# Kernel tuning notes

Hardware: AMD Instinct MI355X
Metric: run time of the kernel (lower is better)

## Reference

```python
import jax, jax.numpy as jnp
import numpy as np

B = 65536      # batch
FDIM = 256     # features_dim (flatten extractor => obs dim)
ADIM = 8       # action dim
T = 3          # n_tasks
H = 256        # net_arch width
IN = FDIM + ADIM

_PARAM_SHAPES = [("W1", (T, IN, H)), ("b1", (T, H)), ("W2", (T, H, H)), ("b2", (T, H)),
                 ("W3", (T, H, H)), ("b3", (T, H)), ("W4", (T, H, 1)), ("b4", (T, 1))]

def setup_inputs() -> dict:
    key = jax.random.key(0)
    ks = jax.random.split(key, 2 + 2 * len(_PARAM_SHAPES))
    d = {"obs": jax.random.normal(ks[0], (B, FDIM), dtype=jnp.float32),
         "actions": jax.random.normal(ks[1], (B, ADIM), dtype=jnp.float32)}
    i = 2
    for q in ("q1", "q2"):
        for name, sh in _PARAM_SHAPES:
            d[f"{q}_{name}"] = jax.random.normal(ks[i], sh, dtype=jnp.float32) * 0.05
            i += 1
    return d

def _heads(x, W1, b1, W2, b2, W3, b3, W4, b4):
    # x: [B, IN]; per-task stacked MLP -> [T, B]
    h = jax.nn.relu(jnp.einsum('bi,tih->tbh', x, W1) + b1[:, None, :])
    h = jax.nn.relu(jnp.einsum('tbh,thk->tbk', h, W2) + b2[:, None, :])
    h = jax.nn.relu(jnp.einsum('tbh,thk->tbk', h, W3) + b3[:, None, :])
    return (jnp.einsum('tbh,tho->tbo', h, W4) + b4[:, None, :])[..., 0]

def reference(obs, actions,
              q1_W1, q1_b1, q1_W2, q1_b2, q1_W3, q1_b3, q1_W4, q1_b4,
              q2_W1, q2_b1, q2_W2, q2_b2, q2_W3, q2_b3, q2_W4, q2_b4):
    x = jnp.concatenate([obs, actions], axis=1)           # [B, IN]
    task = jnp.argmax(obs[:, -T:], axis=-1)               # [B] hard top-1 routing
    mask = jax.nn.one_hot(task, T, dtype=x.dtype).T       # [T, B]
    y1 = _heads(x, q1_W1, q1_b1, q1_W2, q1_b2, q1_W3, q1_b3, q1_W4, q1_b4)  # [T, B]
    y2 = _heads(x, q2_W1, q2_b1, q2_W2, q2_b2, q2_W3, q2_b3, q2_W4, q2_b4)
    q1 = jnp.sum(y1 * mask, axis=0)[:, None]              # [B, 1]
    q2 = jnp.sum(y2 * mask, axis=0)[:, None]
    return (q1, q2)
```

## Files before the change

### kernel.cpp

```cpp
#include <hip/hip_runtime.h>
#include <hip/hip_bf16.h>


#define NB 65536
#define MROWS 48
#define XSTR 296
#define HSTR 264

typedef __attribute__((ext_vector_type(8))) short short8;
typedef __attribute__((ext_vector_type(4))) short short4v;
typedef __attribute__((ext_vector_type(4))) float f32x4;

__device__ __forceinline__ float bf2f(unsigned short u){
  union { unsigned int i; float f; } x; x.i = ((unsigned int)u) << 16; return x.f;
}
__device__ __forceinline__ unsigned short f2bf(float f){
  unsigned int x = __float_as_uint(f);
  x += 0x7fffu + ((x >> 16) & 1u);
  return (unsigned short)(x >> 16);
}
__device__ __forceinline__ float ldval(const void* p, int idx, int isbf16){
  return isbf16 ? bf2f(((const unsigned short*)p)[idx]) : ((const float*)p)[idx];
}

__device__ __forceinline__ int block_sniff(const void* obs, int tid, int* sflag){
  if (tid < 64) {
    unsigned short u = ((const unsigned short*)obs)[tid * 2];
    int e = (u >> 7) & 0xFF;
    unsigned long long m = __ballot(e >= 110 && e <= 132);
    if (tid == 0) *sflag = (__popcll(m) >= 32) ? 1 : 0;
  }
  __syncthreads();
  return *sflag;
}

struct KParams {
  const void* obs;
  const void* act;
  const unsigned short* w1t[2];
  const unsigned short* w2t[2];
  const unsigned short* w3t[2];
  const void* b1[2];
  const void* b2[2];
  const void* b3[2];
  const void* w4[2];
  const void* b4[2];
  const int* counts;
  const int* perm;
  void* out;
};

__device__ __forceinline__ int task_of(const void* obs, int b, int isbf16){
  float v0, v1, v2;
  if (isbf16) {
    short4v u = *(const short4v*)((const unsigned short*)obs + b * 256 + 252);
    v0 = bf2f((unsigned short)u[1]); v1 = bf2f((unsigned short)u[2]); v2 = bf2f((unsigned short)u[3]);
  } else {
    f32x4 u = *(const f32x4*)((const float*)obs + b * 256 + 252);
    v0 = u[1]; v1 = u[2]; v2 = u[3];
  }
  int t = 0; float m = v0;
  if (v1 > m) { m = v1; t = 1; }
  if (v2 > m) { t = 2; }
  return t;
}

__global__ void prep_count(const void* q1W1, const void* q1W2, const void* q1W3,
                           const void* q2W1, const void* q2W2, const void* q2W3,
                           const void* obs, unsigned short* out,
                           int* hist, unsigned char* tasks){
  __shared__ int sflag;
  int tid = threadIdx.x;
  int isbf16 = block_sniff(obs, tid, &sflag);
  if (blockIdx.x >= 600) {
    __shared__ int h[3];
    if (tid < 3) h[tid] = 0;
    __syncthreads();
    int blk = blockIdx.x - 600;
    int b = blk * 256 + tid;
    int t = task_of(obs, b, isbf16);
    tasks[b] = (unsigned char)t;
    atomicAdd(&h[t], 1);
    __syncthreads();
    if (tid < 3) hist[blk * 3 + tid] = h[tid];
    return;
  }
  int gid8 = (blockIdx.x * 256 + tid) * 8;
  int net = gid8 / 614400;
  int idx = gid8 - net * 614400;
  const void* W1 = net ? q2W1 : q1W1;
  const void* W2 = net ? q2W2 : q1W2;
  const void* W3 = net ? q2W3 : q1W3;
  short8 sv;
  if (idx < 221184) {
    int t = idx / 73728; int i = idx - t * 73728;
    int g = i / 4608;  int r = i - g * 4608;
    int kb = r >> 9;   int q2 = r & 511;
    int l16 = q2 >> 5; int rem = q2 & 31;
    int n = g * 16 + l16;
    int k = kb * 32 + (rem & ~7);
    #pragma unroll
    for (int j = 0; j < 8; j++) {
      int kk = k + j;
      sv[j] = (kk < 264) ? (short)f2bf(ldval(W1, (t * 264 + kk) * 256 + n, isbf16)) : (short)0;
    }
  } else if (idx < 417792) {
    int j0 = idx - 221184;
    int t = j0 >> 16; int i = j0 & 65535;
    int g = i >> 12;  int r = i & 4095;
    int kb = r >> 9;  int q2 = r & 511;
    int l16 = q2 >> 5; int rem = q2 & 31;
    int n = g * 16 + l16;
    int k = kb * 32 + (rem & ~7);
    #pragma unroll
    for (int j = 0; j < 8; j++)
      sv[j] = (short)f2bf(ldval(W2, t * 65536 + (k + j) * 256 + n, isbf16));
  } else {
    int j0 = idx - 417792;
    int t = j0 >> 16; int i = j0 & 65535;
    int g = i >> 12;  int r = i & 4095;
    int kb = r >> 9;  int q2 = r & 511;
    int l16 = q2 >> 5; int rem = q2 & 31;
    int n = g * 16 + l16;
    int k = kb * 32 + (rem & ~7);
    #pragma unroll
    for (int j = 0; j < 8; j++)
      sv[j] = (short)f2bf(ldval(W3, t * 65536 + (k + j) * 256 + n, isbf16));
  }
  *(short8*)(out + net * 614400 + idx) = sv;
}

__global__ void route_scatter(const unsigned char* __restrict__ tasks,
                              const int* __restrict__ hist,
                              int* counts, int* perm){
  __shared__ int sh[3][256];
  __shared__ int totals[3], pres[3], base[3], zz[3];
  int tid = threadIdx.x;
  int blk = blockIdx.x;
  sh[0][tid] = hist[tid * 3 + 0];
  sh[1][tid] = hist[tid * 3 + 1];
  sh[2][tid] = hist[tid * 3 + 2];
  if (tid < 3) zz[tid] = 0;
  __syncthreads();
  if (tid < 3) {
    int tot = 0, pre = 0;
    for (int b = 0; b < 256; b++) {
      int v = sh[tid][b];
      if (b < blk) pre += v;
      tot += v;
    }
    totals[tid] = tot; pres[tid] = pre;
  }
  __syncthreads();
  if (tid < 3) {
    int a0 = ((totals[0] + MROWS - 1) / MROWS) * MROWS;
    int a1 = ((totals[1] + MROWS - 1) / MROWS) * MROWS;
    int off = (tid == 0) ? 0 : (tid == 1) ? a0 : a0 + a1;
    base[tid] = off + pres[tid];
    if (blk == 0) counts[tid] = totals[tid];
  }
  __syncthreads();
  int b = blk * 256 + tid;
  int t = tasks[b];
  int r = atomicAdd(&zz[t], 1);
  perm[base[t] + r] = b;
}

template<int KC>
__device__ __forceinline__ void run_layer(const unsigned short* __restrict__ lin, int lstride,
                                          const unsigned short* __restrict__ wt,
                                          const void* bias, unsigned short* lout,
                                          int isbf16, int wave, int quad, int l16, int nbase){
  const unsigned short* wg = wt + (wave * 2) * (KC * 512) + l16 * 32 + quad * 8;
  short8 bfr[KC][2];
  #pragma unroll
  for (int kb = 0; kb < KC; ++kb) {
    bfr[kb][0] = *(const short8*)(wg + kb * 512);
    bfr[kb][1] = *(const short8*)(wg + KC * 512 + kb * 512);
  }
  f32x4 acc[3][2] = {};
  #pragma unroll
  for (int kb = 0; kb < KC; ++kb) {
    short8 afr[3];
    int ko = kb * 32 + quad * 8;
    #pragma unroll
    for (int mt = 0; mt < 3; mt++)
      afr[mt] = *(const short8*)(lin + (mt * 16 + l16) * lstride + ko);
    #pragma unroll
    for (int mt = 0; mt < 3; mt++)
      #pragma unroll
      for (int nt = 0; nt < 2; nt++)
        acc[mt][nt] = __builtin_amdgcn_mfma_f32_16x16x32_bf16(afr[mt], bfr[kb][nt], acc[mt][nt], 0, 0, 0);
  }
  float bv[2];
  #pragma unroll
  for (int nt = 0; nt < 2; nt++) bv[nt] = ldval(bias, nbase + nt * 16 + l16, isbf16);
  #pragma unroll
  for (int mt = 0; mt < 3; mt++)
    #pragma unroll
    for (int nt = 0; nt < 2; nt++) {
      f32x4 a = acc[mt][nt];
      #pragma unroll
      for (int r = 0; r < 4; r++) {
        float v = fmaxf(a[r] + bv[nt], 0.f);
        lout[(mt * 16 + quad * 4 + r) * HSTR + nbase + nt * 16 + l16] = f2bf(v);
      }
    }
  __syncthreads();
}

__global__ __launch_bounds__(512, 6) void fused_kernel(KParams p){
  __shared__ unsigned short X[MROWS * XSTR];
  __shared__ unsigned short HA[MROWS * HSTR];
  unsigned short* HB = X;
  int* sflag = (int*)HA;

  int tid = threadIdx.x;
  int net = blockIdx.y;
  int p0  = blockIdx.x * MROWS;
  int isbf16 = block_sniff(p.obs, tid, sflag);
  int c0 = p.counts[0], c1 = p.counts[1], c2 = p.counts[2];
  int off1 = ((c0 + MROWS - 1) / MROWS) * MROWS;
  int off2 = off1 + ((c1 + MROWS - 1) / MROWS) * MROWS;
  int task  = (p0 >= off2) ? 2 : ((p0 >= off1) ? 1 : 0);
  int segend = (task == 0) ? c0 : (task == 1) ? off1 + c1 : off2 + c2;

  if (tid < MROWS * 8) {
    int srow = tid >> 3, seg = tid & 7;
    int pos = p0 + srow;
    int r = (pos < segend) ? p.perm[pos] : -1;
    #pragma unroll
    for (int j = 0; j < 5; ++j) {
      int c = seg + 8 * j;
      if (c <= 35) {
        short8 sv = {0,0,0,0,0,0,0,0};
        if (r >= 0 && c < 33) {
          if (isbf16) {
            const unsigned short* src = (c < 32) ? ((const unsigned short*)p.obs + r * 256 + c * 8)
                                                 : ((const unsigned short*)p.act + r * 8);
            sv = *(const short8*)src;
          } else {
            const float* src = (c < 32) ? ((const float*)p.obs + r * 256 + c * 8)
                                        : ((const float*)p.act + r * 8);
            f32x4 a = *(const f32x4*)src;
            f32x4 b = *(const f32x4*)(src + 4);
            #pragma unroll
            for (int q = 0; q < 4; q++) { sv[q] = (short)f2bf(a[q]); sv[4 + q] = (short)f2bf(b[q]); }
          }
        }
        *(short8*)(X + srow * XSTR + c * 8) = sv;
      }
    }
  }
  __syncthreads();

  int wave = tid >> 6, lane = tid & 63, quad = lane >> 4, l16 = lane & 15;
  int nbase = wave * 32;

  int bsz = isbf16 ? 2 : 4;
  run_layer<9>(X,  XSTR, p.w1t[net] + task * 73728, (const char*)p.b1[net] + task * 256 * bsz, HA, isbf16, wave, quad, l16, nbase);
  run_layer<8>(HA, HSTR, p.w2t[net] + task * 65536, (const char*)p.b2[net] + task * 256 * bsz, HB, isbf16, wave, quad, l16, nbase);
  run_layer<8>(HB, HSTR, p.w3t[net] + task * 65536, (const char*)p.b3[net] + task * 256 * bsz, HA, isbf16, wave, quad, l16, nbase);

  if (tid < MROWS * 8) {
    int row = tid >> 3, seg = tid & 7;
    float s = 0.f;
    #pragma unroll
    for (int kk = 0; kk < 32; kk += 8) {
      short8 hv = *(const short8*)(HA + row * HSTR + seg * 32 + kk);
      float wv[8];
      if (isbf16) {
        const unsigned short* w4p = (const unsigned short*)p.w4[net] + task * 256 + seg * 32 + kk;
        short8 t = *(const short8*)w4p;
        #pragma unroll
        for (int j = 0; j < 8; j++) wv[j] = bf2f((unsigned short)t[j]);
      } else {
        const float* w4p = (const float*)p.w4[net] + task * 256 + seg * 32 + kk;
        f32x4 a = *(const f32x4*)w4p;
        f32x4 b = *(const f32x4*)(w4p + 4);
        #pragma unroll
        for (int j = 0; j < 4; j++) { wv[j] = a[j]; wv[4 + j] = b[j]; }
      }
      #pragma unroll
      for (int j = 0; j < 8; j++)
        s += bf2f((unsigned short)hv[j]) * wv[j];
    }
    s += __shfl_xor(s, 1);
    s += __shfl_xor(s, 2);
    s += __shfl_xor(s, 4);
    if (seg == 0) {
      int pos = p0 + row;
      if (pos < segend) {
        int r = p.perm[pos];
        float y = s + ldval(p.b4[net], task, isbf16);
        if (isbf16) ((unsigned short*)p.out)[net * NB + r] = f2bf(y);
        else        ((float*)p.out)[net * NB + r] = y;
      }
    }
  }
}

extern "C" void kernel_launch(void* const* d_in, const int* in_sizes, int n_in,
                              void* d_out, int out_size, void* d_ws, size_t ws_size,
                              hipStream_t stream) {
  char* ws = (char*)d_ws;
  int* counts  = (int*)ws;
  int* hist    = (int*)(ws + 64);
  unsigned char* tasks = (unsigned char*)(ws + 3200);
  int* perm    = (int*)(ws + 68800);
  unsigned short* wts  = (unsigned short*)(ws + 331520);

  const void* obs = d_in[0];
  const void* act = d_in[1];

  prep_count<<<856, 256, 0, stream>>>(d_in[2], d_in[4], d_in[6],
                                      d_in[10], d_in[12], d_in[14],
                                      obs, wts, hist, tasks);
  route_scatter<<<256, 256, 0, stream>>>(tasks, hist, counts, perm);

  KParams kp;
  kp.obs = obs; kp.act = act;
  for (int q = 0; q < 2; q++) {
    int base = 2 + q * 8;
    kp.b1[q] = d_in[base + 1];
    kp.b2[q] = d_in[base + 3];
    kp.b3[q] = d_in[base + 5];
    kp.w4[q] = d_in[base + 6];
    kp.b4[q] = d_in[base + 7];
    kp.w1t[q] = wts + q * 614400;
    kp.w2t[q] = wts + q * 614400 + 221184;
    kp.w3t[q] = wts + q * 614400 + 417792;
  }
  kp.counts = counts; kp.perm = perm;
  kp.out = d_out;

  fused_kernel<<<dim3(1368, 2), 512, 0, stream>>>(kp);
}
```

Baseline: 222.4 us.

## Prefetch next-layer weights into registers during MFMA and grow row tile to 64

Splits each layer into a weight-fragment load, an MFMA pass and an epilogue, so the next layer's weight fragments (and biases, W4) are fetched from global memory while the current layer's MFMAs and epilogue run. The first layer's weights are loaded before the input gather. The row tile grows from 48 to 64 rows, which cuts the grid size and amortizes weight loads over more rows, and occupancy is lowered to 4 blocks per CU to fit the extra registers. More register pressure and more padding waste per task segment are the trade-offs.

```diff
diff --git a/kernel.cpp b/kernel.cpp
--- a/kernel.cpp
+++ b/kernel.cpp
@@ -3,7 +3,7 @@
 
 
 #define NB 65536
-#define MROWS 48
+#define MROWS 64
 #define XSTR 296
 #define HSTR 264
 
@@ -166,50 +166,57 @@
   perm[base[t] + r] = b;
 }
 
+template<int KC> struct BF { short8 v[KC][2]; };
+
 template<int KC>
-__device__ __forceinline__ void run_layer(const unsigned short* __restrict__ lin, int lstride,
-                                          const unsigned short* __restrict__ wt,
-                                          const void* bias, unsigned short* lout,
-                                          int isbf16, int wave, int quad, int l16, int nbase){
+__device__ __forceinline__ void load_bf(BF<KC>& f, const unsigned short* __restrict__ wt,
+                                        int wave, int quad, int l16){
   const unsigned short* wg = wt + (wave * 2) * (KC * 512) + l16 * 32 + quad * 8;
-  short8 bfr[KC][2];
   #pragma unroll
   for (int kb = 0; kb < KC; ++kb) {
-    bfr[kb][0] = *(const short8*)(wg + kb * 512);
-    bfr[kb][1] = *(const short8*)(wg + KC * 512 + kb * 512);
-  }
-  f32x4 acc[3][2] = {};
+    f.v[kb][0] = *(const short8*)(wg + kb * 512);
+    f.v[kb][1] = *(const short8*)(wg + KC * 512 + kb * 512);
+  }
+}
+
+template<int KC>
+__device__ __forceinline__ void mfma_layer(const unsigned short* __restrict__ lin, int lstride,
+                                           const BF<KC>& f, f32x4 acc[4][2],
+                                           int quad, int l16){
+  const f32x4 z = {0.f, 0.f, 0.f, 0.f};
   #pragma unroll
   for (int kb = 0; kb < KC; ++kb) {
-    short8 afr[3];
+    short8 afr[4];
     int ko = kb * 32 + quad * 8;
     #pragma unroll
-    for (int mt = 0; mt < 3; mt++)
+    for (int mt = 0; mt < 4; mt++)
       afr[mt] = *(const short8*)(lin + (mt * 16 + l16) * lstride + ko);
     #pragma unroll
-    for (int mt = 0; mt < 3; mt++)
+    for (int mt = 0; mt < 4; mt++)
       #pragma unroll
       for (int nt = 0; nt < 2; nt++)
-        acc[mt][nt] = __builtin_amdgcn_mfma_f32_16x16x32_bf16(afr[mt], bfr[kb][nt], acc[mt][nt], 0, 0, 0);
-  }
-  float bv[2];
+        acc[mt][nt] = __builtin_amdgcn_mfma_f32_16x16x32_bf16(
+            afr[mt], f.v[kb][nt], (kb == 0) ? z : acc[mt][nt], 0, 0, 0);
+  }
+}
+
+__device__ __forceinline__ void epilogue(f32x4 acc[4][2], float bv0, float bv1,
+                                         unsigned short* lout, int quad, int l16, int nbase){
   #pragma unroll
-  for (int nt = 0; nt < 2; nt++) bv[nt] = ldval(bias, nbase + nt * 16 + l16, isbf16);
-  #pragma unroll
-  for (int mt = 0; mt < 3; mt++)
+  for (int mt = 0; mt < 4; mt++)
     #pragma unroll
     for (int nt = 0; nt < 2; nt++) {
+      float bv = nt ? bv1 : bv0;
       f32x4 a = acc[mt][nt];
       #pragma unroll
       for (int r = 0; r < 4; r++) {
-        float v = fmaxf(a[r] + bv[nt], 0.f);
+        float v = fmaxf(a[r] + bv, 0.f);
         lout[(mt * 16 + quad * 4 + r) * HSTR + nbase + nt * 16 + l16] = f2bf(v);
       }
     }
-  __syncthreads();
-}
-
-__global__ __launch_bounds__(512, 6) void fused_kernel(KParams p){
+}
+
+__global__ __launch_bounds__(512, 4) void fused_kernel(KParams p){
   __shared__ unsigned short X[MROWS * XSTR];
   __shared__ unsigned short HA[MROWS * HSTR];
   unsigned short* HB = X;
@@ -218,14 +225,22 @@
   int tid = threadIdx.x;
   int net = blockIdx.y;
   int p0  = blockIdx.x * MROWS;
-  int isbf16 = block_sniff(p.obs, tid, sflag);
+  int wave = tid >> 6, lane = tid & 63, quad = lane >> 4, l16 = lane & 15;
+  int nbase = wave * 32;
+
   int c0 = p.counts[0], c1 = p.counts[1], c2 = p.counts[2];
   int off1 = ((c0 + MROWS - 1) / MROWS) * MROWS;
   int off2 = off1 + ((c1 + MROWS - 1) / MROWS) * MROWS;
   int task  = (p0 >= off2) ? 2 : ((p0 >= off1) ? 1 : 0);
   int segend = (task == 0) ? c0 : (task == 1) ? off1 + c1 : off2 + c2;
 
-  if (tid < MROWS * 8) {
+  BF<9> f1;
+  load_bf<9>(f1, p.w1t[net] + task * 73728, wave, quad, l16);
+
+  int isbf16 = block_sniff(p.obs, tid, sflag);
+  int bsz = isbf16 ? 2 : 4;
+
+  {
     int srow = tid >> 3, seg = tid & 7;
     int pos = p0 + srow;
     int r = (pos < segend) ? p.perm[pos] : -1;
@@ -254,36 +269,62 @@
   }
   __syncthreads();
 
-  int wave = tid >> 6, lane = tid & 63, quad = lane >> 4, l16 = lane & 15;
-  int nbase = wave * 32;
-
-  int bsz = isbf16 ? 2 : 4;
-  run_layer<9>(X,  XSTR, p.w1t[net] + task * 73728, (const char*)p.b1[net] + task * 256 * bsz, HA, isbf16, wave, quad, l16, nbase);
-  run_layer<8>(HA, HSTR, p.w2t[net] + task * 65536, (const char*)p.b2[net] + task * 256 * bsz, HB, isbf16, wave, quad, l16, nbase);
-  run_layer<8>(HB, HSTR, p.w3t[net] + task * 65536, (const char*)p.b3[net] + task * 256 * bsz, HA, isbf16, wave, quad, l16, nbase);
-
-  if (tid < MROWS * 8) {
-    int row = tid >> 3, seg = tid & 7;
+  f32x4 acc[4][2];
+
+  const char* b1p = (const char*)p.b1[net] + task * 256 * bsz;
+  float bva0 = ldval(b1p, nbase + l16, isbf16);
+  float bva1 = ldval(b1p, nbase + 16 + l16, isbf16);
+  mfma_layer<9>(X, XSTR, f1, acc, quad, l16);
+  BF<8> f2;
+  load_bf<8>(f2, p.w2t[net] + task * 65536, wave, quad, l16);
+  epilogue(acc, bva0, bva1, HA, quad, l16, nbase);
+  __syncthreads();
+
+  const char* b2p = (const char*)p.b2[net] + task * 256 * bsz;
+  float bvb0 = ldval(b2p, nbase + l16, isbf16);
+  float bvb1 = ldval(b2p, nbase + 16 + l16, isbf16);
+  mfma_layer<8>(HA, HSTR, f2, acc, quad, l16);
+  BF<8> f3;
+  load_bf<8>(f3, p.w3t[net] + task * 65536, wave, quad, l16);
+  epilogue(acc, bvb0, bvb1, HB, quad, l16, nbase);
+  __syncthreads();
+
+  const char* b3p = (const char*)p.b3[net] + task * 256 * bsz;
+  float bvc0 = ldval(b3p, nbase + l16, isbf16);
+  float bvc1 = ldval(b3p, nbase + 16 + l16, isbf16);
+  mfma_layer<8>(HB, HSTR, f3, acc, quad, l16);
+
+  int seg = tid & 7, row = tid >> 3;
+  float wv[32];
+  if (isbf16) {
+    const unsigned short* w4p = (const unsigned short*)p.w4[net] + task * 256 + seg * 32;
+    #pragma unroll
+    for (int q = 0; q < 4; q++) {
+      short8 t = *(const short8*)(w4p + q * 8);
+      #pragma unroll
+      for (int j = 0; j < 8; j++) wv[q * 8 + j] = bf2f((unsigned short)t[j]);
+    }
+  } else {
+    const float* w4p = (const float*)p.w4[net] + task * 256 + seg * 32;
+    #pragma unroll
+    for (int q = 0; q < 8; q++) {
+      f32x4 a = *(const f32x4*)(w4p + q * 4);
+      #pragma unroll
+      for (int j = 0; j < 4; j++) wv[q * 4 + j] = a[j];
+    }
+  }
+  float b4v = ldval(p.b4[net], task, isbf16);
+  epilogue(acc, bvc0, bvc1, HA, quad, l16, nbase);
+  __syncthreads();
+
+  {
     float s = 0.f;
     #pragma unroll
     for (int kk = 0; kk < 32; kk += 8) {
       short8 hv = *(const short8*)(HA + row * HSTR + seg * 32 + kk);
-      float wv[8];
-      if (isbf16) {
-        const unsigned short* w4p = (const unsigned short*)p.w4[net] + task * 256 + seg * 32 + kk;
-        short8 t = *(const short8*)w4p;
-        #pragma unroll
-        for (int j = 0; j < 8; j++) wv[j] = bf2f((unsigned short)t[j]);
-      } else {
-        const float* w4p = (const float*)p.w4[net] + task * 256 + seg * 32 + kk;
-        f32x4 a = *(const f32x4*)w4p;
-        f32x4 b = *(const f32x4*)(w4p + 4);
-        #pragma unroll
-        for (int j = 0; j < 4; j++) { wv[j] = a[j]; wv[4 + j] = b[j]; }
-      }
       #pragma unroll
       for (int j = 0; j < 8; j++)
-        s += bf2f((unsigned short)hv[j]) * wv[j];
+        s += bf2f((unsigned short)hv[j]) * wv[kk + j];
     }
     s += __shfl_xor(s, 1);
     s += __shfl_xor(s, 2);
@@ -292,7 +333,7 @@
       int pos = p0 + row;
       if (pos < segend) {
         int r = p.perm[pos];
-        float y = s + ldval(p.b4[net], task, isbf16);
+        float y = s + b4v;
         if (isbf16) ((unsigned short*)p.out)[net * NB + r] = f2bf(y);
         else        ((float*)p.out)[net * NB + r] = y;
       }
@@ -334,5 +375,5 @@
   kp.counts = counts; kp.perm = perm;
   kp.out = d_out;
 
-  fused_kernel<<<dim3(1368, 2), 512, 0, stream>>>(kp);
-}
+  fused_kernel<<<dim3(1026, 2), 512, 0, stream>>>(kp);
+}
```

New measurement: 215.0 us. 1.03x faster.
